# Kernel tuning notes

Measured on AMD Instinct MI355X. Metric: run time of the kernel, lower is better.

## Reference

```python
import jax, jax.numpy as jnp
import numpy as np

N, E, D_IN, D_OUT, R, B = 50000, 800000, 100, 100, 200, 50
BN_EPS = 1e-5


def setup_inputs() -> dict:
    key = jax.random.key(0)
    ks = jax.random.split(key, 24)
    inv_in = 1.0 / np.sqrt(D_IN)
    lin = lambda k: (jax.random.uniform(k, (D_OUT, D_IN), jnp.float32, -inv_in, inv_in),
                     jax.random.uniform(jax.random.fold_in(k, 1), (D_OUT,), jnp.float32, -inv_in, inv_in))
    Ws_w, Ws_b = lin(ks[0])
    Wk_w, Wk_b = lin(ks[1])
    Wq_w, Wq_b = lin(ks[2])
    Wv_w, Wv_b = lin(ks[3])
    Wr_w, Wr_b = lin(ks[4])
    return {
        "n_in_feats": jax.random.normal(ks[5], (N, D_IN), jnp.float32),
        "r_feats": jax.random.normal(ks[6], (R, D_IN), jnp.float32),
        "src": jax.random.randint(ks[7], (E,), 0, N),
        "dst": jax.random.randint(ks[8], (E,), 0, N),
        "etype": jax.random.randint(ks[9], (E,), 0, R),
        "norm": jax.random.uniform(ks[10], (E, 1), jnp.float32),
        "Ws_w": Ws_w, "Ws_b": Ws_b,
        "Wk_w": Wk_w, "Wk_b": Wk_b,
        "Wq_w": Wq_w, "Wq_b": Wq_b,
        "Wv_w": Wv_w, "Wv_b": Wv_b,
        "Wr_w": Wr_w, "Wr_b": Wr_b,
        "relation_att": jax.random.normal(ks[11], (B, D_OUT), jnp.float32) * np.sqrt(2.0 / (B + D_OUT)),
        "w_comp": jax.random.normal(ks[12], (R, B), jnp.float32) * np.sqrt(2.0 / (R + B)),
        "alpha": jnp.ones((1,), jnp.float32),
        "loop_rel": jax.random.normal(ks[13], (1, D_IN), jnp.float32) * np.sqrt(2.0 / (1 + D_IN)),
        "bn_gamma": jnp.ones((D_OUT,), jnp.float32),
        "bn_beta": jnp.zeros((D_OUT,), jnp.float32),
    }


def reference(n_in_feats, r_feats, src, dst, etype, norm,
              Ws_w, Ws_b, Wk_w, Wk_b, Wq_w, Wq_b, Wv_w, Wv_b, Wr_w, Wr_b,
              relation_att, w_comp, alpha, loop_rel, bn_gamma, bn_beta):
    num_nodes = n_in_feats.shape[0]
    # relation features incl. self-loop relation (appended row)
    r_all = jnp.concatenate([r_feats, loop_rel], axis=0)          # [R+1, D_in]
    # basis-decomposed per-relation attention weights: [R, D_out]
    rel_w = jnp.matmul(w_comp, relation_att)
    # node projections, then gather per edge (edge_attention)
    k = jnp.matmul(n_in_feats, Wk_w.T) + Wk_b                     # [N, D_out]
    q = jnp.matmul(n_in_feats, Wq_w.T) + Wq_b
    v = jnp.matmul(n_in_feats, Wv_w.T) + Wv_b
    k_e = k[src]                                                   # [E, D_out]
    q_e = q[dst]
    v_e = v[src]
    w_e = rel_w[etype]                                             # [E, D_out]
    att = jnp.sum(k_e * w_e * q_e, axis=-1)                       # [E]
    # segment softmax over incoming edges of each dst node
    seg_max = jax.ops.segment_max(att, dst, num_segments=num_nodes)
    e = jnp.exp(att - seg_max[dst])
    denom = jax.ops.segment_sum(e, dst, num_segments=num_nodes)
    att_w = e / denom[dst]                                         # [E]
    final = jax.ops.segment_sum(att_w[:, None] * v_e, dst, num_segments=num_nodes)  # [N, D_out]
    # gated combination (dropout is identity in eval)
    a = jax.nn.sigmoid(alpha[0])
    n_out = a * (jnp.matmul(n_in_feats, Ws_w.T) + Ws_b) + (1.0 - a) * final
    # BatchNorm1d (training-mode batch stats, biased variance)
    mu = jnp.mean(n_out, axis=0)
    var = jnp.mean((n_out - mu) ** 2, axis=0)
    n_out = (n_out - mu) * jax.lax.rsqrt(var + BN_EPS) * bn_gamma + bn_beta
    n_out = jnp.tanh(n_out)
    r_out = jnp.matmul(r_all, Wr_w.T) + Wr_b                      # [R+1, D_out]
    return n_out, r_out[:-1]
```

## Files before the change

kernel.cpp:

```cpp
#include <hip/hip_runtime.h>
#include <hip/hip_bf16.h>
#include <math.h>

#define N_NODES 50000
#define N_EDGES 800000
#define BN_EPS  1e-5f
#define SCAN_NB 49
#define AGG_NB  2048

typedef float floatx2 __attribute__((ext_vector_type(2)));
typedef _Float16 half2_t __attribute__((ext_vector_type(2)));

#if defined(__has_builtin) && __has_builtin(__builtin_amdgcn_fdot2)
#define FDOT2(a, b, c) __builtin_amdgcn_fdot2((a), (b), (c), false)
#else
#define FDOT2(a, b, c) ((c) + (float)(a).x * (float)(b).x + (float)(a).y * (float)(b).y)
#endif

union h2u { half2_t h; unsigned u; };

#define OFS_RELW   0
#define OFS_KH     25600
#define OFS_Q      1625600
#define OFS_VH     8025600
#define OFS_ATTP   9625600
#define OFS_BNPART 10425600
#define OFS_BNSC   10835200
#define OFS_BNSH   10835328
#define OFS_CNT    10835456
#define OFS_PART   10885632
#define OFS_BSUM   10935808
#define OFS_OFFS   10935872
#define OFS_RANK   10986048
#define OFS_PEDGE  11786048
#define OFS_WT     13386048
#define WS_ELEMS   13406848

__global__ __launch_bounds__(256) void prep_kernel(
    const float* __restrict__ wcomp, const float* __restrict__ ratt,
    const float* __restrict__ Wk, const float* __restrict__ Wq,
    const float* __restrict__ Wv, const float* __restrict__ Ws,
    float* __restrict__ relw, unsigned* __restrict__ Wth,
    int* __restrict__ cnt)
{
    const int b = blockIdx.x;
    const int tid = threadIdx.x;
    if (b < 196) {
        int i = b * 256 + tid;
        if (i < 50176) cnt[i] = 0;
    } else if (b < 296) {
        int o = (b - 196) * 256 + tid;
        if (o < 200 * 128) {
            int r = o / 128, c = o % 128;
            float acc = 0.f;
            if (c < 100) {
                #pragma unroll 10
                for (int k = 0; k < 50; ++k)
                    acc += wcomp[r * 50 + k] * ratt[k * 100 + c];
            }
            relw[o] = acc;
        }
    } else {
        int o = (b - 296) * 256 + tid;
        if (o < 4 * 50 * 104) {
            int m = o / 5200, rem = o % 5200, d2 = rem / 104, c = rem % 104;
            const float* W = (m == 0) ? Wk : (m == 1) ? Wq : (m == 2) ? Wv : Ws;
            float a = (c < 100) ? W[c * 100 + 2 * d2]     : 0.f;
            float bb = (c < 100) ? W[c * 100 + 2 * d2 + 1] : 0.f;
            h2u cv; cv.h = half2_t{(_Float16)a, (_Float16)bb};
            Wth[o] = cv.u;
        }
    }
}

__global__ __launch_bounds__(512) void proj_kernel(
    const float* __restrict__ X, const unsigned* __restrict__ Wth,
    const float* __restrict__ bk, const float* __restrict__ bq,
    const float* __restrict__ bv, const float* __restrict__ bs,
    unsigned* __restrict__ khp, float* __restrict__ qo,
    unsigned* __restrict__ vhp, float* __restrict__ so)
{
    __shared__ unsigned Xth[50][68];
    __shared__ unsigned Wlh[50][104];
    const int tid = threadIdx.x;
    const int nb  = blockIdx.x * 64;
    const int m   = blockIdx.y;

    const float* bp = (m == 0) ? bk : (m == 1) ? bq : (m == 2) ? bv : bs;

    for (int idx = tid; idx < 1300; idx += 512) {
        int r = idx / 26, c4 = idx % 26;
        uint4 w = ((const uint4*)(Wth + m * 5200 + r * 104))[c4];
        *(uint4*)&Wlh[r][c4 * 4] = w;
    }
    for (int idx = tid; idx < 1600; idx += 512) {
        int n = idx / 25, d4 = idx % 25;
        int node = nb + n;
        float4 x = (node < N_NODES)
                   ? ((const float4*)(X + (size_t)node * 100))[d4]
                   : make_float4(0.f, 0.f, 0.f, 0.f);
        const int col = n ^ ((d4 & 7) << 2);
        h2u c0, c1;
        c0.h = half2_t{(_Float16)x.x, (_Float16)x.y};
        c1.h = half2_t{(_Float16)x.z, (_Float16)x.w};
        Xth[2 * d4][col]     = c0.u;
        Xth[2 * d4 + 1][col] = c1.u;
    }
    __syncthreads();

    const int nt  = tid & 15;
    const int ct  = tid >> 4;
    const bool act = (ct < 25);
    const int cts  = act ? ct : 24;

    float acc[4][4];
    #pragma unroll
    for (int i = 0; i < 4; ++i)
        #pragma unroll
        for (int j = 0; j < 4; ++j) acc[i][j] = 0.f;

    #pragma unroll 5
    for (int d2 = 0; d2 < 50; ++d2) {
        const int key = ((d2 >> 1) & 7) << 2;
        const uint4 xv = *(const uint4*)&Xth[d2][(4 * nt) ^ key];
        const uint4 wv = *(const uint4*)&Wlh[d2][4 * cts];
        h2u x0, x1, x2, x3, w0, w1, w2, w3;
        x0.u = xv.x; x1.u = xv.y; x2.u = xv.z; x3.u = xv.w;
        w0.u = wv.x; w1.u = wv.y; w2.u = wv.z; w3.u = wv.w;
        acc[0][0] = FDOT2(x0.h, w0.h, acc[0][0]);
        acc[0][1] = FDOT2(x0.h, w1.h, acc[0][1]);
        acc[0][2] = FDOT2(x0.h, w2.h, acc[0][2]);
        acc[0][3] = FDOT2(x0.h, w3.h, acc[0][3]);
        acc[1][0] = FDOT2(x1.h, w0.h, acc[1][0]);
        acc[1][1] = FDOT2(x1.h, w1.h, acc[1][1]);
        acc[1][2] = FDOT2(x1.h, w2.h, acc[1][2]);
        acc[1][3] = FDOT2(x1.h, w3.h, acc[1][3]);
        acc[2][0] = FDOT2(x2.h, w0.h, acc[2][0]);
        acc[2][1] = FDOT2(x2.h, w1.h, acc[2][1]);
        acc[2][2] = FDOT2(x2.h, w2.h, acc[2][2]);
        acc[2][3] = FDOT2(x2.h, w3.h, acc[2][3]);
        acc[3][0] = FDOT2(x3.h, w0.h, acc[3][0]);
        acc[3][1] = FDOT2(x3.h, w1.h, acc[3][1]);
        acc[3][2] = FDOT2(x3.h, w2.h, acc[3][2]);
        acc[3][3] = FDOT2(x3.h, w3.h, acc[3][3]);
    }

    const float4 bb = act ? *(const float4*)(bp + ct * 4)
                          : make_float4(0.f, 0.f, 0.f, 0.f);
    if (m == 0 || m == 2) {
        unsigned* oph = (m == 0) ? khp : vhp;
        #pragma unroll
        for (int i = 0; i < 4; ++i) {
            const int node = nb + nt * 4 + i;
            if (node < N_NODES) {
                unsigned wdo = 0u;
                if (act) {
                    int wd = 0;
                    wd = __builtin_amdgcn_cvt_pk_fp8_f32(
                        acc[i][0] + bb.x, acc[i][1] + bb.y, wd, false);
                    wd = __builtin_amdgcn_cvt_pk_fp8_f32(
                        acc[i][2] + bb.z, acc[i][3] + bb.w, wd, true);
                    wdo = (unsigned)wd;
                }
                oph[(size_t)node * 32 + ct] = wdo;
            }
        }
    } else if (m == 1) {
        #pragma unroll
        for (int i = 0; i < 4; ++i) {
            const int node = nb + nt * 4 + i;
            if (node < N_NODES) {
                float4 r = act ? make_float4(acc[i][0] + bb.x, acc[i][1] + bb.y,
                                             acc[i][2] + bb.z, acc[i][3] + bb.w)
                               : make_float4(0.f, 0.f, 0.f, 0.f);
                *(float4*)(qo + (size_t)node * 128 + ct * 4) = r;
            }
        }
    } else {
        if (act) {
            #pragma unroll
            for (int i = 0; i < 4; ++i) {
                const int node = nb + nt * 4 + i;
                if (node < N_NODES) {
                    float4 r = make_float4(acc[i][0] + bb.x, acc[i][1] + bb.y,
                                           acc[i][2] + bb.z, acc[i][3] + bb.w);
                    *(float4*)(so + (size_t)node * 100 + ct * 4) = r;
                }
            }
        }
    }
}

__global__ __launch_bounds__(256) void hist_kernel(
    const int* __restrict__ dst, int* __restrict__ cnt, int* __restrict__ rank)
{
    int e = blockIdx.x * 256 + threadIdx.x;
    if (e < N_EDGES) rank[e] = atomicAdd(&cnt[dst[e]], 1);
}

__global__ __launch_bounds__(1024) void scanA_kernel(
    const int* __restrict__ cnt, int* __restrict__ partial, int* __restrict__ bsum)
{
    __shared__ int buf[1024];
    int tid = threadIdx.x;
    int i = blockIdx.x * 1024 + tid;
    int val = (i < N_NODES) ? cnt[i] : 0;
    buf[tid] = val;
    __syncthreads();
    for (int off = 1; off < 1024; off <<= 1) {
        int t = (tid >= off) ? buf[tid - off] : 0;
        __syncthreads();
        buf[tid] += t;
        __syncthreads();
    }
    int incl = buf[tid];
    if (i < N_NODES) partial[i] = incl - val;
    if (tid == 1023) bsum[blockIdx.x] = incl;
}

__global__ __launch_bounds__(1024) void scanB_kernel(
    const int* __restrict__ partial, const int* __restrict__ bsum,
    int* __restrict__ offs)
{
    __shared__ int bs[64];
    int tid = threadIdx.x;
    if (tid < SCAN_NB) bs[tid] = bsum[tid];
    __syncthreads();
    if (tid == 0) {
        int run = 0;
        for (int b = 0; b < SCAN_NB; ++b) { int t = bs[b]; bs[b] = run; run += t; }
    }
    __syncthreads();
    for (int i = tid; i < N_NODES; i += 1024) offs[i] = partial[i] + bs[i >> 10];
    if (tid == 0) offs[N_NODES] = N_EDGES;
}

__global__ __launch_bounds__(256) void scatter_kernel(
    const int* __restrict__ src, const int* __restrict__ dst,
    const int* __restrict__ ety, const int* __restrict__ offs,
    const int* __restrict__ rank, unsigned long long* __restrict__ pedge)
{
    int e = blockIdx.x * 256 + threadIdx.x;
    if (e >= N_EDGES) return;
    int d = dst[e];
    pedge[offs[d] + rank[e]] = (unsigned long long)(unsigned)src[e]
                             | ((unsigned long long)(unsigned)ety[e] << 17)
                             | ((unsigned long long)(unsigned)d << 32);
}

__global__ __launch_bounds__(256) void attp_kernel(
    const unsigned* __restrict__ khp, const float* __restrict__ q,
    const float* __restrict__ relw,
    const unsigned long long* __restrict__ pedge, float* __restrict__ attp)
{
    const int lane = threadIdx.x & 15;
    const int i = blockIdx.x * 16 + (threadIdx.x >> 4);
    if (i >= N_EDGES) return;
    const unsigned long long pw = pedge[i];
    const int s_ = (int)(pw & 0x1FFFFull);
    const int t_ = (int)((pw >> 17) & 0x7FFFull);
    const int d_ = (int)(pw >> 32);

    const unsigned* kr = khp + (size_t)s_ * 32;
    const float4*   qr = (const float4*)(q + (size_t)d_ * 128);
    const float4*   wr = (const float4*)(relw + t_ * 128);

    const unsigned kw0 = kr[lane];
    const unsigned kw1 = kr[lane + 16];
    const float4 qv0 = qr[lane];
    const float4 qv1 = qr[lane + 16];
    const float4 wv0 = wr[lane];
    const float4 wv1 = wr[lane + 16];

    const floatx2 ka = __builtin_amdgcn_cvt_pk_f32_fp8((int)kw0, false);
    const floatx2 kb = __builtin_amdgcn_cvt_pk_f32_fp8((int)kw0, true);
    const floatx2 kc = __builtin_amdgcn_cvt_pk_f32_fp8((int)kw1, false);
    const floatx2 kd = __builtin_amdgcn_cvt_pk_f32_fp8((int)kw1, true);

    float acc = ka[0] * wv0.x * qv0.x + ka[1] * wv0.y * qv0.y
              + kb[0] * wv0.z * qv0.z + kb[1] * wv0.w * qv0.w
              + kc[0] * wv1.x * qv1.x + kc[1] * wv1.y * qv1.y
              + kd[0] * wv1.z * qv1.z + kd[1] * wv1.w * qv1.w;

    #pragma unroll
    for (int off = 8; off > 0; off >>= 1) acc += __shfl_xor(acc, off, 16);
    if (lane == 0) attp[i] = __expf(acc);
}

__global__ __launch_bounds__(256) void agg_kernel(
    const int* __restrict__ offs, const unsigned* __restrict__ pedge32,
    const float* __restrict__ attp, const unsigned short* __restrict__ vhp,
    const float* __restrict__ alpha, float* __restrict__ out,
    float* __restrict__ bnpart)
{
    __shared__ float ls[100], lq[100];
    const int tid = threadIdx.x;
    if (tid < 100) { ls[tid] = 0.f; lq[tid] = 0.f; }
    __syncthreads();
    const int lane = tid & 63;
    const int gwave = blockIdx.x * 4 + (tid >> 6);
    const int nwaves = AGG_NB * 4;
    const float a = 1.f / (1.f + __expf(-alpha[0]));
    const float b = 1.f - a;
    const int cl = lane;
    const bool act = (cl < 50);
    float sx = 0.f, sy = 0.f, qx = 0.f, qy = 0.f;

    for (int n = gwave; n < N_NODES; n += nwaves) {
        const int beg = offs[n], end = offs[n + 1];
        float ax = 0.f, ay = 0.f, wsum = 0.f;
        int i = beg;
        for (; i + 4 <= end; i += 4) {
            const int s0 = (int)(pedge32[2 * (i)]     & 0x1FFFFu);
            const int s1 = (int)(pedge32[2 * (i + 1)] & 0x1FFFFu);
            const int s2 = (int)(pedge32[2 * (i + 2)] & 0x1FFFFu);
            const int s3 = (int)(pedge32[2 * (i + 3)] & 0x1FFFFu);
            const float w0 = attp[i],     w1 = attp[i + 1];
            const float w2 = attp[i + 2], w3 = attp[i + 3];
            wsum += w0 + w1 + w2 + w3;
            if (act) {
                const unsigned short h0 = vhp[(size_t)s0 * 64 + cl];
                const unsigned short h1 = vhp[(size_t)s1 * 64 + cl];
                const unsigned short h2 = vhp[(size_t)s2 * 64 + cl];
                const unsigned short h3 = vhp[(size_t)s3 * 64 + cl];
                const floatx2 v0 = __builtin_amdgcn_cvt_pk_f32_fp8((int)h0, false);
                const floatx2 v1 = __builtin_amdgcn_cvt_pk_f32_fp8((int)h1, false);
                const floatx2 v2 = __builtin_amdgcn_cvt_pk_f32_fp8((int)h2, false);
                const floatx2 v3 = __builtin_amdgcn_cvt_pk_f32_fp8((int)h3, false);
                ax += w0 * v0[0] + w1 * v1[0] + w2 * v2[0] + w3 * v3[0];
                ay += w0 * v0[1] + w1 * v1[1] + w2 * v2[1] + w3 * v3[1];
            }
        }
        for (; i < end; ++i) {
            const int s0 = (int)(pedge32[2 * i] & 0x1FFFFu);
            const float w0 = attp[i];
            wsum += w0;
            if (act) {
                const unsigned short h0 = vhp[(size_t)s0 * 64 + cl];
                const floatx2 v0 = __builtin_amdgcn_cvt_pk_f32_fp8((int)h0, false);
                ax += w0 * v0[0];
                ay += w0 * v0[1];
            }
        }
        const float inv = (wsum > 0.f) ? 1.f / wsum : 0.f;
        if (act) {
            float2* po = (float2*)(out + (size_t)n * 100);
            float2 cur = po[cl];
            float v0 = a * cur.x + b * ax * inv;
            float v1 = a * cur.y + b * ay * inv;
            po[cl] = make_float2(v0, v1);
            sx += v0; qx += v0 * v0;
            sy += v1; qy += v1 * v1;
        }
    }
    if (act) {
        atomicAdd(&ls[2 * cl], sx);     atomicAdd(&ls[2 * cl + 1], sy);
        atomicAdd(&lq[2 * cl], qx);     atomicAdd(&lq[2 * cl + 1], qy);
    }
    __syncthreads();
    if (tid < 100) {
        bnpart[(size_t)tid * AGG_NB + blockIdx.x]         = ls[tid];
        bnpart[(size_t)(tid + 100) * AGG_NB + blockIdx.x] = lq[tid];
    }
}

__global__ __launch_bounds__(256) void bnfin_kernel(
    const float* __restrict__ bnpart,
    const float* __restrict__ gamma, const float* __restrict__ beta,
    float* __restrict__ bnsc, float* __restrict__ bnsh)
{
    const int c = blockIdx.x * 4 + (threadIdx.x >> 6);
    const int lane = threadIdx.x & 63;
    if (c >= 100) return;
    float s = 0.f, q = 0.f;
    for (int b2 = lane; b2 < AGG_NB; b2 += 64) {
        s += bnpart[(size_t)c * AGG_NB + b2];
        q += bnpart[(size_t)(c + 100) * AGG_NB + b2];
    }
    #pragma unroll
    for (int off = 32; off > 0; off >>= 1) {
        s += __shfl_xor(s, off, 64);
        q += __shfl_xor(q, off, 64);
    }
    if (lane == 0) {
        const float inv_n = 1.f / (float)N_NODES;
        float mean = s * inv_n;
        float var = q * inv_n - mean * mean;
        float sc = gamma[c] * rsqrtf(var + BN_EPS);
        bnsc[c] = sc;
        bnsh[c] = beta[c] - mean * sc;
    }
}

__global__ __launch_bounds__(256) void applyrout_kernel(
    float* __restrict__ out, const float* __restrict__ bnsc,
    const float* __restrict__ bnsh,
    const float* __restrict__ rf, const float* __restrict__ Wr,
    const float* __restrict__ br)
{
    if (blockIdx.x < 2048) {
        const int total4 = N_NODES * 25;
        for (int idx = blockIdx.x * 256 + threadIdx.x; idx < total4; idx += 2048 * 256) {
            float4* p = ((float4*)out) + idx;
            const int c = (idx % 25) * 4;
            float4 t = *p;
            t.x = tanhf(t.x * bnsc[c]     + bnsh[c]);
            t.y = tanhf(t.y * bnsc[c + 1] + bnsh[c + 1]);
            t.z = tanhf(t.z * bnsc[c + 2] + bnsh[c + 2]);
            t.w = tanhf(t.w * bnsc[c + 3] + bnsh[c + 3]);
            *p = t;
        }
    } else {
        int o = (blockIdx.x - 2048) * 256 + threadIdx.x;
        if (o < 200 * 100) {
            int r = o / 100, c = o % 100;
            float acc = br[c];
            #pragma unroll 10
            for (int d = 0; d < 100; ++d) acc += rf[r * 100 + d] * Wr[c * 100 + d];
            out[N_NODES * 100 + o] = acc;
        }
    }
}

extern "C" void kernel_launch(void* const* d_in, const int* in_sizes, int n_in,
                              void* d_out, int out_size, void* d_ws, size_t ws_size,
                              hipStream_t stream) {
    const float* X     = (const float*)d_in[0];
    const float* rfeat = (const float*)d_in[1];
    const int*   src   = (const int*)d_in[2];
    const int*   dst   = (const int*)d_in[3];
    const int*   ety   = (const int*)d_in[4];
    const float* Wsw   = (const float*)d_in[6];
    const float* Wsb   = (const float*)d_in[7];
    const float* Wkw   = (const float*)d_in[8];
    const float* Wkb   = (const float*)d_in[9];
    const float* Wqw   = (const float*)d_in[10];
    const float* Wqb   = (const float*)d_in[11];
    const float* Wvw   = (const float*)d_in[12];
    const float* Wvb   = (const float*)d_in[13];
    const float* Wrw   = (const float*)d_in[14];
    const float* Wrb   = (const float*)d_in[15];
    const float* ratt  = (const float*)d_in[16];
    const float* wcomp = (const float*)d_in[17];
    const float* alpha = (const float*)d_in[18];
    const float* gamma = (const float*)d_in[20];
    const float* beta  = (const float*)d_in[21];

    float* out = (float*)d_out;
    float* ws  = (float*)d_ws;
    if (ws_size < (size_t)WS_ELEMS * sizeof(float)) return;

    float* relw          = ws + OFS_RELW;
    unsigned* khp        = (unsigned*)(ws + OFS_KH);
    float* q             = ws + OFS_Q;
    unsigned* vhp        = (unsigned*)(ws + OFS_VH);
    float* attp          = ws + OFS_ATTP;
    float* bnpart        = ws + OFS_BNPART;
    float* bnsc          = ws + OFS_BNSC;
    float* bnsh          = ws + OFS_BNSH;
    unsigned* Wth        = (unsigned*)(ws + OFS_WT);
    int* cnt             = (int*)(ws + OFS_CNT);
    int* partial         = (int*)(ws + OFS_PART);
    int* bsum            = (int*)(ws + OFS_BSUM);
    int* offs            = (int*)(ws + OFS_OFFS);
    int* rank            = (int*)(ws + OFS_RANK);
    unsigned long long* pedge = (unsigned long long*)(ws + OFS_PEDGE);

    prep_kernel<<<196 + 100 + 82, 256, 0, stream>>>(
        wcomp, ratt, Wkw, Wqw, Wvw, Wsw, relw, Wth, cnt);
    proj_kernel<<<dim3((N_NODES + 63) / 64, 4), 512, 0, stream>>>(
        X, Wth, Wkb, Wqb, Wvb, Wsb, khp, q, vhp, out);

    hist_kernel<<<(N_EDGES + 255) / 256, 256, 0, stream>>>(dst, cnt, rank);
    scanA_kernel<<<SCAN_NB, 1024, 0, stream>>>(cnt, partial, bsum);
    scanB_kernel<<<1, 1024, 0, stream>>>(partial, bsum, offs);
    scatter_kernel<<<(N_EDGES + 255) / 256, 256, 0, stream>>>(
        src, dst, ety, offs, rank, pedge);

    attp_kernel<<<(N_EDGES + 15) / 16, 256, 0, stream>>>(
        khp, q, relw, pedge, attp);
    agg_kernel<<<AGG_NB, 256, 0, stream>>>(
        offs, (const unsigned*)pedge, attp, (const unsigned short*)vhp,
        alpha, out, bnpart);
    bnfin_kernel<<<25, 256, 0, stream>>>(bnpart, gamma, beta, bnsc, bnsh);
    applyrout_kernel<<<2048 + (20000 + 255) / 256, 256, 0, stream>>>(
        out, bnsc, bnsh, rfeat, Wrw, Wrb);
}
```

Before: 233.4 us.

## Fuse edge attention scoring into aggregation and interleave K/V rows

Removes the separate per-edge attention kernel and computes the score inside the per-destination aggregation wave: each wave loads q once per node, gathers the fp8 K half-row and relation weights, reduces with a 64-lane shuffle, and exponentiates inline. K and V are stored interleaved in one 256-byte row per node so one gather locality serves both. Edge records shrink from 64-bit to 32-bit because the destination is implicit. This drops the attp write/read and the 64-bit pedge traffic, but adds serial shuffle-reduction latency per edge pair inside the aggregation loop, and inactive lanes (cl>=50) now read padding.

```diff
diff --git a/kernel.cpp b/kernel.cpp
--- a/kernel.cpp
+++ b/kernel.cpp
@@ -20,21 +20,19 @@
 union h2u { half2_t h; unsigned u; };
 
 #define OFS_RELW   0
-#define OFS_KH     25600
-#define OFS_Q      1625600
-#define OFS_VH     8025600
-#define OFS_ATTP   9625600
-#define OFS_BNPART 10425600
-#define OFS_BNSC   10835200
-#define OFS_BNSH   10835328
-#define OFS_CNT    10835456
-#define OFS_PART   10885632
-#define OFS_BSUM   10935808
-#define OFS_OFFS   10935872
-#define OFS_RANK   10986048
-#define OFS_PEDGE  11786048
-#define OFS_WT     13386048
-#define WS_ELEMS   13406848
+#define OFS_KVP    25600
+#define OFS_Q      3225600
+#define OFS_BNPART 9625600
+#define OFS_BNSC   10035200
+#define OFS_BNSH   10035328
+#define OFS_CNT    10035456
+#define OFS_PART   10085632
+#define OFS_BSUM   10135808
+#define OFS_OFFS   10135872
+#define OFS_RANK   10186048
+#define OFS_PEDGE  10986048
+#define OFS_WT     11786048
+#define WS_ELEMS   11806848
 
 __global__ __launch_bounds__(256) void prep_kernel(
     const float* __restrict__ wcomp, const float* __restrict__ ratt,
@@ -77,8 +75,8 @@
     const float* __restrict__ X, const unsigned* __restrict__ Wth,
     const float* __restrict__ bk, const float* __restrict__ bq,
     const float* __restrict__ bv, const float* __restrict__ bs,
-    unsigned* __restrict__ khp, float* __restrict__ qo,
-    unsigned* __restrict__ vhp, float* __restrict__ so)
+    unsigned* __restrict__ kvp, float* __restrict__ qo,
+    float* __restrict__ so)
 {
     __shared__ unsigned Xth[50][68];
     __shared__ unsigned Wlh[50][104];
@@ -148,7 +146,7 @@
     const float4 bb = act ? *(const float4*)(bp + ct * 4)
                           : make_float4(0.f, 0.f, 0.f, 0.f);
     if (m == 0 || m == 2) {
-        unsigned* oph = (m == 0) ? khp : vhp;
+        const int wofs = (m == 0) ? ct : (32 + ct);
         #pragma unroll
         for (int i = 0; i < 4; ++i) {
             const int node = nb + nt * 4 + i;
@@ -162,7 +160,7 @@
                         acc[i][2] + bb.z, acc[i][3] + bb.w, wd, true);
                     wdo = (unsigned)wd;
                 }
-                oph[(size_t)node * 32 + ct] = wdo;
+                kvp[(size_t)node * 64 + wofs] = wdo;
             }
         }
     } else if (m == 1) {
@@ -238,60 +236,19 @@
 __global__ __launch_bounds__(256) void scatter_kernel(
     const int* __restrict__ src, const int* __restrict__ dst,
     const int* __restrict__ ety, const int* __restrict__ offs,
-    const int* __restrict__ rank, unsigned long long* __restrict__ pedge)
+    const int* __restrict__ rank, unsigned* __restrict__ pedge)
 {
     int e = blockIdx.x * 256 + threadIdx.x;
     if (e >= N_EDGES) return;
     int d = dst[e];
-    pedge[offs[d] + rank[e]] = (unsigned long long)(unsigned)src[e]
-                             | ((unsigned long long)(unsigned)ety[e] << 17)
-                             | ((unsigned long long)(unsigned)d << 32);
-}
-
-__global__ __launch_bounds__(256) void attp_kernel(
-    const unsigned* __restrict__ khp, const float* __restrict__ q,
-    const float* __restrict__ relw,
-    const unsigned long long* __restrict__ pedge, float* __restrict__ attp)
-{
-    const int lane = threadIdx.x & 15;
-    const int i = blockIdx.x * 16 + (threadIdx.x >> 4);
-    if (i >= N_EDGES) return;
-    const unsigned long long pw = pedge[i];
-    const int s_ = (int)(pw & 0x1FFFFull);
-    const int t_ = (int)((pw >> 17) & 0x7FFFull);
-    const int d_ = (int)(pw >> 32);
-
-    const unsigned* kr = khp + (size_t)s_ * 32;
-    const float4*   qr = (const float4*)(q + (size_t)d_ * 128);
-    const float4*   wr = (const float4*)(relw + t_ * 128);
-
-    const unsigned kw0 = kr[lane];
-    const unsigned kw1 = kr[lane + 16];
-    const float4 qv0 = qr[lane];
-    const float4 qv1 = qr[lane + 16];
-    const float4 wv0 = wr[lane];
-    const float4 wv1 = wr[lane + 16];
-
-    const floatx2 ka = __builtin_amdgcn_cvt_pk_f32_fp8((int)kw0, false);
-    const floatx2 kb = __builtin_amdgcn_cvt_pk_f32_fp8((int)kw0, true);
-    const floatx2 kc = __builtin_amdgcn_cvt_pk_f32_fp8((int)kw1, false);
-    const floatx2 kd = __builtin_amdgcn_cvt_pk_f32_fp8((int)kw1, true);
-
-    float acc = ka[0] * wv0.x * qv0.x + ka[1] * wv0.y * qv0.y
-              + kb[0] * wv0.z * qv0.z + kb[1] * wv0.w * qv0.w
-              + kc[0] * wv1.x * qv1.x + kc[1] * wv1.y * qv1.y
-              + kd[0] * wv1.z * qv1.z + kd[1] * wv1.w * qv1.w;
-
-    #pragma unroll
-    for (int off = 8; off > 0; off >>= 1) acc += __shfl_xor(acc, off, 16);
-    if (lane == 0) attp[i] = __expf(acc);
+    pedge[offs[d] + rank[e]] = (unsigned)src[e] | ((unsigned)ety[e] << 17);
 }
 
 __global__ __launch_bounds__(256) void agg_kernel(
-    const int* __restrict__ offs, const unsigned* __restrict__ pedge32,
-    const float* __restrict__ attp, const unsigned short* __restrict__ vhp,
-    const float* __restrict__ alpha, float* __restrict__ out,
-    float* __restrict__ bnpart)
+    const int* __restrict__ offs, const unsigned* __restrict__ pedge,
+    const unsigned* __restrict__ kvp, const float* __restrict__ q,
+    const float* __restrict__ relw, const float* __restrict__ alpha,
+    float* __restrict__ out, float* __restrict__ bnpart)
 {
     __shared__ float ls[100], lq[100];
     const int tid = threadIdx.x;
@@ -304,43 +261,57 @@
     const float b = 1.f - a;
     const int cl = lane;
     const bool act = (cl < 50);
+    const unsigned short* kv16 = (const unsigned short*)kvp;
     float sx = 0.f, sy = 0.f, qx = 0.f, qy = 0.f;
 
     for (int n = gwave; n < N_NODES; n += nwaves) {
         const int beg = offs[n], end = offs[n + 1];
+        const float2 qv = ((const float2*)(q + (size_t)n * 128))[cl];
         float ax = 0.f, ay = 0.f, wsum = 0.f;
         int i = beg;
-        for (; i + 4 <= end; i += 4) {
-            const int s0 = (int)(pedge32[2 * (i)]     & 0x1FFFFu);
-            const int s1 = (int)(pedge32[2 * (i + 1)] & 0x1FFFFu);
-            const int s2 = (int)(pedge32[2 * (i + 2)] & 0x1FFFFu);
-            const int s3 = (int)(pedge32[2 * (i + 3)] & 0x1FFFFu);
-            const float w0 = attp[i],     w1 = attp[i + 1];
-            const float w2 = attp[i + 2], w3 = attp[i + 3];
-            wsum += w0 + w1 + w2 + w3;
-            if (act) {
-                const unsigned short h0 = vhp[(size_t)s0 * 64 + cl];
-                const unsigned short h1 = vhp[(size_t)s1 * 64 + cl];
-                const unsigned short h2 = vhp[(size_t)s2 * 64 + cl];
-                const unsigned short h3 = vhp[(size_t)s3 * 64 + cl];
-                const floatx2 v0 = __builtin_amdgcn_cvt_pk_f32_fp8((int)h0, false);
-                const floatx2 v1 = __builtin_amdgcn_cvt_pk_f32_fp8((int)h1, false);
-                const floatx2 v2 = __builtin_amdgcn_cvt_pk_f32_fp8((int)h2, false);
-                const floatx2 v3 = __builtin_amdgcn_cvt_pk_f32_fp8((int)h3, false);
-                ax += w0 * v0[0] + w1 * v1[0] + w2 * v2[0] + w3 * v3[0];
-                ay += w0 * v0[1] + w1 * v1[1] + w2 * v2[1] + w3 * v3[1];
+        for (; i + 2 <= end; i += 2) {
+            const unsigned p0 = pedge[i], p1 = pedge[i + 1];
+            const int s0 = (int)(p0 & 0x1FFFFu), t0 = (int)(p0 >> 17);
+            const int s1 = (int)(p1 & 0x1FFFFu), t1 = (int)(p1 >> 17);
+            const unsigned short* r0 = kv16 + (size_t)s0 * 128;
+            const unsigned short* r1 = kv16 + (size_t)s1 * 128;
+            const unsigned short kh0 = r0[cl],      kh1 = r1[cl];
+            const unsigned short vh0 = r0[64 + cl], vh1 = r1[64 + cl];
+            const float2 wv0 = ((const float2*)(relw + t0 * 128))[cl];
+            const float2 wv1 = ((const float2*)(relw + t1 * 128))[cl];
+            const floatx2 k0 = __builtin_amdgcn_cvt_pk_f32_fp8((int)kh0, false);
+            const floatx2 k1 = __builtin_amdgcn_cvt_pk_f32_fp8((int)kh1, false);
+            float pa = k0[0] * wv0.x * qv.x + k0[1] * wv0.y * qv.y;
+            float pb = k1[0] * wv1.x * qv.x + k1[1] * wv1.y * qv.y;
+            #pragma unroll
+            for (int off = 32; off > 0; off >>= 1) {
+                pa += __shfl_xor(pa, off, 64);
+                pb += __shfl_xor(pb, off, 64);
             }
+            const float w0 = __expf(pa), w1 = __expf(pb);
+            wsum += w0 + w1;
+            const floatx2 v0 = __builtin_amdgcn_cvt_pk_f32_fp8((int)vh0, false);
+            const floatx2 v1 = __builtin_amdgcn_cvt_pk_f32_fp8((int)vh1, false);
+            ax += w0 * v0[0] + w1 * v1[0];
+            ay += w0 * v0[1] + w1 * v1[1];
         }
         for (; i < end; ++i) {
-            const int s0 = (int)(pedge32[2 * i] & 0x1FFFFu);
-            const float w0 = attp[i];
+            const unsigned p0 = pedge[i];
+            const int s0 = (int)(p0 & 0x1FFFFu), t0 = (int)(p0 >> 17);
+            const unsigned short* r0 = kv16 + (size_t)s0 * 128;
+            const unsigned short kh0 = r0[cl];
+            const unsigned short vh0 = r0[64 + cl];
+            const float2 wv0 = ((const float2*)(relw + t0 * 128))[cl];
+            const floatx2 k0 = __builtin_amdgcn_cvt_pk_f32_fp8((int)kh0, false);
+            float pa = k0[0] * wv0.x * qv.x + k0[1] * wv0.y * qv.y;
+            #pragma unroll
+            for (int off = 32; off > 0; off >>= 1)
+                pa += __shfl_xor(pa, off, 64);
+            const float w0 = __expf(pa);
             wsum += w0;
-            if (act) {
-                const unsigned short h0 = vhp[(size_t)s0 * 64 + cl];
-                const floatx2 v0 = __builtin_amdgcn_cvt_pk_f32_fp8((int)h0, false);
-                ax += w0 * v0[0];
-                ay += w0 * v0[1];
-            }
+            const floatx2 v0 = __builtin_amdgcn_cvt_pk_f32_fp8((int)vh0, false);
+            ax += w0 * v0[0];
+            ay += w0 * v0[1];
         }
         const float inv = (wsum > 0.f) ? 1.f / wsum : 0.f;
         if (act) {
@@ -451,10 +422,8 @@
     if (ws_size < (size_t)WS_ELEMS * sizeof(float)) return;
 
     float* relw          = ws + OFS_RELW;
-    unsigned* khp        = (unsigned*)(ws + OFS_KH);
+    unsigned* kvp        = (unsigned*)(ws + OFS_KVP);
     float* q             = ws + OFS_Q;
-    unsigned* vhp        = (unsigned*)(ws + OFS_VH);
-    float* attp          = ws + OFS_ATTP;
     float* bnpart        = ws + OFS_BNPART;
     float* bnsc          = ws + OFS_BNSC;
     float* bnsh          = ws + OFS_BNSH;
@@ -464,12 +433,12 @@
     int* bsum            = (int*)(ws + OFS_BSUM);
     int* offs            = (int*)(ws + OFS_OFFS);
     int* rank            = (int*)(ws + OFS_RANK);
-    unsigned long long* pedge = (unsigned long long*)(ws + OFS_PEDGE);
+    unsigned* pedge      = (unsigned*)(ws + OFS_PEDGE);
 
     prep_kernel<<<196 + 100 + 82, 256, 0, stream>>>(
         wcomp, ratt, Wkw, Wqw, Wvw, Wsw, relw, Wth, cnt);
     proj_kernel<<<dim3((N_NODES + 63) / 64, 4), 512, 0, stream>>>(
-        X, Wth, Wkb, Wqb, Wvb, Wsb, khp, q, vhp, out);
+        X, Wth, Wkb, Wqb, Wvb, Wsb, kvp, q, out);
 
     hist_kernel<<<(N_EDGES + 255) / 256, 256, 0, stream>>>(dst, cnt, rank);
     scanA_kernel<<<SCAN_NB, 1024, 0, stream>>>(cnt, partial, bsum);
@@ -477,11 +446,8 @@
     scatter_kernel<<<(N_EDGES + 255) / 256, 256, 0, stream>>>(
         src, dst, ety, offs, rank, pedge);
 
-    attp_kernel<<<(N_EDGES + 15) / 16, 256, 0, stream>>>(
-        khp, q, relw, pedge, attp);
     agg_kernel<<<AGG_NB, 256, 0, stream>>>(
-        offs, (const unsigned*)pedge, attp, (const unsigned short*)vhp,
-        alpha, out, bnpart);
+        offs, pedge, kvp, q, relw, alpha, out, bnpart);
     bnfin_kernel<<<25, 256, 0, stream>>>(bnpart, gamma, beta, bnsc, bnsh);
     applyrout_kernel<<<2048 + (20000 + 255) / 256, 256, 0, stream>>>(
         out, bnsc, bnsh, rfeat, Wrw, Wrb);
```

After: 233.9 us. About the same (+0.2%).
